# Kernel tuning notes

Measured on AMD Instinct MI355X. Metric: run time of the kernel, lower is better.

The kernel has to match this reference:

```python
import jax, jax.numpy as jnp
import numpy as np

# Dimensions
O, D, F_LSOA = 128, 128, 64      # origins, destinations, LSOA feature dim
T, FE, H = 128, 16, 64           # max seq len, edge_feature_dim, gru_hidden
NH, NO, PH = 128, 64, 128        # node_hidden, node_out, pair_hidden
P = O * D                        # number of O-D pairs


def _mlp3(x, W1, b1, W2, b2, W3, b3):
    # Linear->ReLU->Linear->ReLU->Linear (dropout is identity in eval mode)
    h = jax.nn.relu(x @ W1 + b1)
    h = jax.nn.relu(h @ W2 + b2)
    return h @ W3 + b3


def setup_inputs() -> dict:
    key = jax.random.key(0)
    ks = jax.random.split(key, 32)

    def rn(k, shape, s):
        return jax.random.normal(k, shape, dtype=jnp.float32) * s

    inp = {
        "O_feats": rn(ks[0], (O, F_LSOA), 1.0),
        "D_feats": rn(ks[1], (D, F_LSOA), 1.0),
        "seqs": rn(ks[2], (P, T, FE), 1.0),
        "lengths": jax.random.randint(ks[3], (P,), 1, T + 1, dtype=jnp.int32),
        # enc_O
        "WO1": rn(ks[4], (F_LSOA, NH), 0.05), "bO1": jnp.zeros((NH,), jnp.float32),
        "WO2": rn(ks[5], (NH, NH), 0.05),     "bO2": jnp.zeros((NH,), jnp.float32),
        "WO3": rn(ks[6], (NH, NO), 0.05),     "bO3": jnp.zeros((NO,), jnp.float32),
        # enc_D
        "WD1": rn(ks[7], (F_LSOA, NH), 0.05), "bD1": jnp.zeros((NH,), jnp.float32),
        "WD2": rn(ks[8], (NH, NH), 0.05),     "bD2": jnp.zeros((NH,), jnp.float32),
        "WD3": rn(ks[9], (NH, NO), 0.05),     "bD3": jnp.zeros((NO,), jnp.float32),
        # pair_head: 2*node_out -> pair_hidden -> 1
        "Wp1": rn(ks[10], (2 * NO, PH), 0.05), "bp1": jnp.zeros((PH,), jnp.float32),
        "Wp2": rn(ks[11], (PH, 1), 0.05),      "bp2": jnp.zeros((1,), jnp.float32),
        # GRU (gate order r, z, n as in PyTorch)
        "W_ih": rn(ks[12], (FE, 3 * H), 0.1),  "b_ih": jnp.zeros((3 * H,), jnp.float32),
        "W_hh": rn(ks[13], (H, 3 * H), 0.1),   "b_hh": jnp.zeros((3 * H,), jnp.float32),
        # seq_head
        "Ws": rn(ks[14], (H, 1), 0.1),         "bs": jnp.zeros((1,), jnp.float32),
    }
    return inp


def reference(O_feats, D_feats, seqs, lengths,
              WO1, bO1, WO2, bO2, WO3, bO3,
              WD1, bD1, WD2, bD2, WD3, bD3,
              Wp1, bp1, Wp2, bp2,
              W_ih, W_hh, b_ih, b_hh,
              Ws, bs):
    # Node encoders
    eo = _mlp3(O_feats, WO1, bO1, WO2, bO2, WO3, bO3)   # [O, NO]
    ed = _mlp3(D_feats, WD1, bD1, WD2, bD2, WD3, bD3)   # [D, NO]

    # Pairwise score: concat(eo, ed) -> MLP -> softplus
    pair_in = jnp.concatenate([
        jnp.broadcast_to(eo[:, None, :], (O, D, NO)),
        jnp.broadcast_to(ed[None, :, :], (O, D, NO)),
    ], axis=-1)                                          # [O, D, 2*NO]
    hp = jax.nn.relu(pair_in @ Wp1 + bp1)                # [O, D, PH]
    z_pair = (hp @ Wp2 + bp2)[..., 0]                    # [O, D]
    s_pair = jax.nn.softplus(z_pair)

    # Length-masked GRU over all O*D padded sequences (equiv. to pack_padded)
    xT = jnp.swapaxes(seqs, 0, 1)                        # [T, P, FE]
    h0 = jnp.zeros((P, H), jnp.float32)

    def step(h, inp):
        xt, t = inp
        gx = xt @ W_ih + b_ih                            # [P, 3H]
        gh = h @ W_hh + b_hh                             # [P, 3H]
        xr, xz, xn = jnp.split(gx, 3, axis=-1)
        hr, hz, hn = jnp.split(gh, 3, axis=-1)
        r = jax.nn.sigmoid(xr + hr)
        zg = jax.nn.sigmoid(xz + hz)
        n = jnp.tanh(xn + r * hn)
        h_new = (1.0 - zg) * n + zg * h
        h = jnp.where((t < lengths)[:, None], h_new, h)  # freeze past seq end
        return h, None

    h_last, _ = jax.lax.scan(step, h0, (xT, jnp.arange(T)))  # [P, H]

    p_seq = jax.nn.sigmoid(h_last @ Ws + bs)[:, 0].reshape(O, D)
    return jnp.sum(s_pair * p_seq)
```

## Files before the change

### kernel.cpp

```cpp
#include <hip/hip_runtime.h>
#include <hip/hip_bf16.h>

#define O_N 128
#define D_N 128
#define F_LS 64
#define T_MAX 128
#define FE_N 16
#define H_GRU 64
#define NH 128
#define NO 64
#define PH 128

typedef _Float16 f16;
typedef __fp16 hf2 __attribute__((ext_vector_type(2)));
typedef f16 f16x4 __attribute__((ext_vector_type(4)));
typedef f16 f16x8 __attribute__((ext_vector_type(8)));
typedef float f32x4 __attribute__((ext_vector_type(4)));

__device__ __forceinline__ float fast_sigmoid(float x) {
    return __builtin_amdgcn_rcpf(1.f + __expf(-x));
}

__global__ __launch_bounds__(256) void k_pre(
    const float* __restrict__ O_feats, const float* __restrict__ D_feats,
    const float* __restrict__ WO1, const float* __restrict__ bO1,
    const float* __restrict__ WO2, const float* __restrict__ bO2,
    const float* __restrict__ WO3, const float* __restrict__ bO3,
    const float* __restrict__ WD1, const float* __restrict__ bD1,
    const float* __restrict__ WD2, const float* __restrict__ bD2,
    const float* __restrict__ WD3, const float* __restrict__ bD3,
    const float* __restrict__ Wp1, const float* __restrict__ bp1,
    const int* __restrict__ lengths,
    float* __restrict__ PA, float* __restrict__ PBt,
    int* __restrict__ perm, float* __restrict__ d_out)
{
    const int t = threadIdx.x;
    if (blockIdx.x == 256) {
        __shared__ int cnt[130];
        __shared__ int suf[130];
        if (t < 130) cnt[t] = 0;
        __syncthreads();
        for (int i = t; i < 16384; i += 256) atomicAdd(&cnt[lengths[i]], 1);
        __syncthreads();
        if (t < 130) suf[t] = cnt[t];
        __syncthreads();
        for (int d = 1; d < 130; d <<= 1) {
            int v = 0;
            if (t < 130) { v = suf[t]; if (t + d < 130) v += suf[t + d]; }
            __syncthreads();
            if (t < 130) suf[t] = v;
            __syncthreads();
        }
        if (t < 129) cnt[t] = (t + 1 < 130) ? suf[t + 1] : 0;
        __syncthreads();
        for (int i = t; i < 16384; i += 256) {
            int pos = atomicAdd(&cnt[lengths[i]], 1);
            perm[pos] = i;
        }
        return;
    }

    __shared__ float h1[NH];
    __shared__ float h2[NH];
    __shared__ float ev[NO];
    const int b = blockIdx.x;
    const int enc = b >> 7;
    const int row = b & 127;
    if (b == 0 && t == 0) d_out[0] = 0.f;

    const float* x  = (enc ? D_feats : O_feats) + row * F_LS;
    const float* W1 = enc ? WD1 : WO1;  const float* b1 = enc ? bD1 : bO1;
    const float* W2 = enc ? WD2 : WO2;  const float* b2 = enc ? bD2 : bO2;
    const float* W3 = enc ? WD3 : WO3;  const float* b3 = enc ? bD3 : bO3;

    if (t < 128) {
        float a = b1[t];
        #pragma unroll 8
        for (int k = 0; k < F_LS; ++k) a += x[k] * W1[k * NH + t];
        h1[t] = fmaxf(a, 0.f);
    }
    __syncthreads();

    if (t < 128) {
        float a = b2[t];
        #pragma unroll 8
        for (int k = 0; k < NH; ++k) a += h1[k] * W2[k * NH + t];
        h2[t] = fmaxf(a, 0.f);
    }
    __syncthreads();

    if (t < NO) {
        float a = b3[t];
        #pragma unroll 8
        for (int k = 0; k < NH; ++k) a += h2[k] * W3[k * NO + t];
        ev[t] = a;
    }
    __syncthreads();

    if (t < 128) {
        const float* Wp = Wp1 + (enc ? NO * PH : 0);
        float a = 0.f;
        #pragma unroll 8
        for (int k = 0; k < NO; ++k) a += ev[k] * Wp[k * PH + t];
        if (enc) PBt[t * 128 + row] = a + bp1[t];
        else     PA[row * PH + t] = a;
    }
}

__global__ __launch_bounds__(256, 4) void k_gru(
    const float* __restrict__ seqs, const int* __restrict__ lengths,
    const int* __restrict__ perm,
    const float* __restrict__ W_ih, const float* __restrict__ b_ih,
    const float* __restrict__ W_hh, const float* __restrict__ b_hh,
    const float* __restrict__ Ws, const float* __restrict__ bs,
    const float* __restrict__ PA, const float* __restrict__ PBt,
    const float* __restrict__ Wp2, const float* __restrict__ bp2,
    float* __restrict__ d_out)
{
    __shared__ __align__(16) f16 hbuf[2][16 * 72];
    __shared__ __align__(16) float4 xbuf[2][8][64];
    __shared__ float red[64];
    const int tid = threadIdx.x;
    const int w  = tid >> 6;
    const int l  = tid & 63;
    const int q  = l >> 4;
    const int n  = l & 15;
    const int c  = w * 16 + n;
    const int colbase = w * 16 + q * 4;
    const int b2 = blockIdx.x & 255;
    const int j  = blockIdx.x >> 8;
    const int g  = (j == 0) ? 2 * b2
                 : (j == 1) ? 2 * b2 + 1
                 : (j == 2) ? 1022 - 2 * b2
                            : 1023 - 2 * b2;
    const int pb = g * 16;
    const float S_RZ = -1.4426950408889634f;
    const float S_N  =  2.8853900817779268f;

    f16x8 wh[3][2], wi[3];
    #pragma unroll
    for (int gg = 0; gg < 3; ++gg) {
        const int gb = gg * 64;
        const float s = (gg < 2) ? S_RZ : S_N;
        #pragma unroll
        for (int ks = 0; ks < 2; ++ks)
            #pragma unroll
            for (int jj = 0; jj < 8; ++jj)
                wh[gg][ks][jj] = (f16)(W_hh[(ks * 32 + q * 8 + jj) * 192 + gb + c] * s);
        #pragma unroll
        for (int jj = 0; jj < 8; ++jj) {
            int k = q * 8 + jj;
            wi[gg][jj] = (k < FE_N) ? (f16)(W_ih[k * 192 + gb + c] * s) : (f16)0.f;
        }
    }
    f32x4 c_r, c_z, c_hn, c_xn;
    float wsc[4];
    #pragma unroll
    for (int r = 0; r < 4; ++r) {
        int col = colbase + r;
        c_r[r]  = S_RZ * (b_ih[col] + b_hh[col]);
        c_z[r]  = S_RZ * (b_ih[64 + col] + b_hh[64 + col]);
        c_hn[r] = S_N * b_hh[128 + col];
        c_xn[r] = S_N * b_ih[128 + col];
        wsc[r]  = Ws[col];
    }
    const int myp   = perm[pb + n];
    const int mylen = lengths[myp];
    int ml = mylen;
    ml = max(ml, __shfl_xor(ml, 1));
    ml = max(ml, __shfl_xor(ml, 2));
    ml = max(ml, __shfl_xor(ml, 4));
    ml = max(ml, __shfl_xor(ml, 8));
    const int maxlen = __builtin_amdgcn_readfirstlane(ml);

    const float* xsrc = seqs + (size_t)perm[pb + (l & 15)] * (T_MAX * FE_N)
                       + (l >> 4) * 4;

    if (tid < 144) { f16x8 z8 = {}; *(f16x8*)&hbuf[0][tid * 8] = z8; }

    #pragma unroll
    for (int rr = 0; rr < 2; ++rr) {
        const int r8 = w + rr * 4;
        __builtin_amdgcn_global_load_lds(
            (const __attribute__((address_space(1))) void*)(xsrc + (size_t)r8 * FE_N),
            (__attribute__((address_space(3))) void*)&xbuf[0][r8][0], 16, 0, 0);
    }
    float hold[4] = {0.f, 0.f, 0.f, 0.f};
    const f16x8 zero8 = {};
    __syncthreads();

    #pragma unroll 1
    for (int t = 0; t < maxlen; ++t) {
        const int cur = t & 1;
        const int xb  = (t >> 3) & 1;
        const int row = t & 7;
        const f16* hb  = hbuf[cur];
        f16*       hbw = hbuf[cur ^ 1];
        f16x8 bh0 = *(const f16x8*)&hb[n * 72 + 8 * q];
        f16x8 bh1 = *(const f16x8*)&hb[n * 72 + 32 + 8 * q];

        if (row == 0 && t + 8 < maxlen) {
            const int nb = xb ^ 1;
            #pragma unroll
            for (int rr = 0; rr < 2; ++rr) {
                const int rl = w + rr * 4;
                int rg = t + 8 + rl;
                rg = rg < T_MAX ? rg : T_MAX - 1;
                __builtin_amdgcn_global_load_lds(
                    (const __attribute__((address_space(1))) void*)(xsrc + (size_t)rg * FE_N),
                    (__attribute__((address_space(3))) void*)&xbuf[nb][rl][0], 16, 0, 0);
            }
        }

        f16x8 ax = zero8;
        if (q < 2) {
            float4 a0 = xbuf[xb][row][32 * q + n];
            float4 a1 = xbuf[xb][row][32 * q + 16 + n];
            union { f16x8 v8; hf2 v2[4]; } u;
            u.v2[0] = __builtin_amdgcn_cvt_pkrtz(a0.x, a0.y);
            u.v2[1] = __builtin_amdgcn_cvt_pkrtz(a0.z, a0.w);
            u.v2[2] = __builtin_amdgcn_cvt_pkrtz(a1.x, a1.y);
            u.v2[3] = __builtin_amdgcn_cvt_pkrtz(a1.z, a1.w);
            ax = u.v8;
        }

        f32x4 ar = __builtin_amdgcn_mfma_f32_16x16x32_f16(wi[0], ax, c_r, 0, 0, 0);
        f32x4 az = __builtin_amdgcn_mfma_f32_16x16x32_f16(wi[1], ax, c_z, 0, 0, 0);
        f32x4 xn = __builtin_amdgcn_mfma_f32_16x16x32_f16(wi[2], ax, c_xn, 0, 0, 0);
        ar = __builtin_amdgcn_mfma_f32_16x16x32_f16(wh[0][0], bh0, ar, 0, 0, 0);
        ar = __builtin_amdgcn_mfma_f32_16x16x32_f16(wh[0][1], bh1, ar, 0, 0, 0);
        az = __builtin_amdgcn_mfma_f32_16x16x32_f16(wh[1][0], bh0, az, 0, 0, 0);
        az = __builtin_amdgcn_mfma_f32_16x16x32_f16(wh[1][1], bh1, az, 0, 0, 0);
        f32x4 hn = __builtin_amdgcn_mfma_f32_16x16x32_f16(wh[2][0], bh0, c_hn, 0, 0, 0);
        hn = __builtin_amdgcn_mfma_f32_16x16x32_f16(wh[2][1], bh1, hn, 0, 0, 0);

        const bool live = (t < mylen);
        #pragma unroll
        for (int r = 0; r < 4; ++r) {
            float rg    = __builtin_amdgcn_rcpf(1.f + __builtin_amdgcn_exp2f(ar[r]));
            float zg    = __builtin_amdgcn_rcpf(1.f + __builtin_amdgcn_exp2f(az[r]));
            float inner = fmaf(rg, hn[r], xn[r]);
            float nn    = fmaf(-2.f, __builtin_amdgcn_rcpf(1.f + __builtin_amdgcn_exp2f(inner)), 1.f);
            float hnew  = fmaf(zg, hold[r] - nn, nn);
            hold[r] = live ? hnew : hold[r];
        }
        union { f16x4 v4; hf2 v2[2]; } hu;
        hu.v2[0] = __builtin_amdgcn_cvt_pkrtz(hold[0], hold[1]);
        hu.v2[1] = __builtin_amdgcn_cvt_pkrtz(hold[2], hold[3]);
        *(f16x4*)&hbw[n * 72 + colbase] = hu.v4;
        __syncthreads();
    }

    float part = hold[0] * wsc[0] + hold[1] * wsc[1] +
                 hold[2] * wsc[2] + hold[3] * wsc[3];
    part += __shfl_xor(part, 16);
    part += __shfl_xor(part, 32);
    if (l < 16) red[w * 16 + n] = part;
    __syncthreads();

    const int pp = tid >> 4;
    const int u  = tid & 15;
    const int pidx = perm[pb + pp];
    const int ii = pidx >> 7;
    const int jj = pidx & 127;
    float acc = 0.f;
    #pragma unroll
    for (int cc = u; cc < PH; cc += 16)
        acc += Wp2[cc] * fmaxf(PA[ii * PH + cc] + PBt[cc * 128 + jj], 0.f);
    acc += __shfl_xor(acc, 1);
    acc += __shfl_xor(acc, 2);
    acc += __shfl_xor(acc, 4);
    acc += __shfl_xor(acc, 8);
    float contrib = 0.f;
    if (u == 0) {
        float z  = acc + bp2[0];
        float sp = fmaxf(z, 0.f) + log1pf(__expf(-fabsf(z)));
        float s  = red[pp] + red[16 + pp] + red[32 + pp] + red[48 + pp];
        float pv = fast_sigmoid(s + bs[0]);
        contrib  = sp * pv;
    }
    __syncthreads();
    if (u == 0) red[pp] = contrib;
    __syncthreads();
    if (tid == 0) {
        float tot = 0.f;
        #pragma unroll
        for (int k = 0; k < 16; ++k) tot += red[k];
        atomicAdd(d_out, tot);
    }
}

extern "C" void kernel_launch(void* const* d_in, const int* in_sizes, int n_in,
                              void* d_out, int out_size, void* d_ws, size_t ws_size,
                              hipStream_t stream)
{
    const float* O_feats = (const float*)d_in[0];
    const float* D_feats = (const float*)d_in[1];
    const float* seqs    = (const float*)d_in[2];
    const int*   lengths = (const int*)d_in[3];
    const float* WO1 = (const float*)d_in[4];  const float* bO1 = (const float*)d_in[5];
    const float* WO2 = (const float*)d_in[6];  const float* bO2 = (const float*)d_in[7];
    const float* WO3 = (const float*)d_in[8];  const float* bO3 = (const float*)d_in[9];
    const float* WD1 = (const float*)d_in[10]; const float* bD1 = (const float*)d_in[11];
    const float* WD2 = (const float*)d_in[12]; const float* bD2 = (const float*)d_in[13];
    const float* WD3 = (const float*)d_in[14]; const float* bD3 = (const float*)d_in[15];
    const float* Wp1 = (const float*)d_in[16]; const float* bp1 = (const float*)d_in[17];
    const float* Wp2 = (const float*)d_in[18]; const float* bp2 = (const float*)d_in[19];
    const float* W_ih = (const float*)d_in[20]; const float* b_ih = (const float*)d_in[21];
    const float* W_hh = (const float*)d_in[22]; const float* b_hh = (const float*)d_in[23];
    const float* Ws   = (const float*)d_in[24]; const float* bs   = (const float*)d_in[25];

    float* out    = (float*)d_out;
    float* PA     = (float*)d_ws;
    float* PBt    = PA + 128 * 128;
    int*   perm   = (int*)(PBt + 128 * 128);

    k_pre<<<257, 256, 0, stream>>>(O_feats, D_feats,
                                   WO1, bO1, WO2, bO2, WO3, bO3,
                                   WD1, bD1, WD2, bD2, WD3, bD3,
                                   Wp1, bp1, lengths, PA, PBt, perm, out);
    k_gru<<<1024, 256, 0, stream>>>(seqs, lengths, perm, W_ih, b_ih, W_hh, b_hh,
                                    Ws, bs, PA, PBt, Wp2, bp2, out);
}
```

Baseline: 341.6 us.

## Convert GRU kernel to persistent blocks pulling length-sorted groups from an atomic queue

The GRU kernel becomes persistent. 512 blocks repeatedly claim 16-sequence groups from a global atomic counter, which k_pre resets. Because perm is sorted by descending length, this gives dynamic longest-first scheduling. Each group's maxlen is read from its first element instead of a shuffle reduction, and per-pair results go straight to the output with atomicAdd, replacing the per-block reduction. The aim is load balancing across uneven sequence lengths. In exchange, far fewer blocks are resident to hide recurrence latency, and there are more global atomics.

```diff
diff --git a/kernel.cpp b/kernel.cpp
--- a/kernel.cpp
+++ b/kernel.cpp
@@ -10,6 +10,7 @@
 #define NH 128
 #define NO 64
 #define PH 128
+#define NGRP 1024
 
 typedef _Float16 f16;
 typedef __fp16 hf2 __attribute__((ext_vector_type(2)));
@@ -32,12 +33,13 @@
     const float* __restrict__ Wp1, const float* __restrict__ bp1,
     const int* __restrict__ lengths,
     float* __restrict__ PA, float* __restrict__ PBt,
-    int* __restrict__ perm, float* __restrict__ d_out)
+    int* __restrict__ perm, int* __restrict__ gcnt, float* __restrict__ d_out)
 {
     const int t = threadIdx.x;
     if (blockIdx.x == 256) {
         __shared__ int cnt[130];
         __shared__ int suf[130];
+        if (t == 0) gcnt[0] = 0;
         if (t < 130) cnt[t] = 0;
         __syncthreads();
         for (int i = t; i < 16384; i += 256) atomicAdd(&cnt[lengths[i]], 1);
@@ -109,7 +111,7 @@
 
 __global__ __launch_bounds__(256, 4) void k_gru(
     const float* __restrict__ seqs, const int* __restrict__ lengths,
-    const int* __restrict__ perm,
+    const int* __restrict__ perm, int* __restrict__ gcnt,
     const float* __restrict__ W_ih, const float* __restrict__ b_ih,
     const float* __restrict__ W_hh, const float* __restrict__ b_hh,
     const float* __restrict__ Ws, const float* __restrict__ bs,
@@ -120,6 +122,7 @@
     __shared__ __align__(16) f16 hbuf[2][16 * 72];
     __shared__ __align__(16) float4 xbuf[2][8][64];
     __shared__ float red[64];
+    __shared__ int sg;
     const int tid = threadIdx.x;
     const int w  = tid >> 6;
     const int l  = tid & 63;
@@ -127,13 +130,6 @@
     const int n  = l & 15;
     const int c  = w * 16 + n;
     const int colbase = w * 16 + q * 4;
-    const int b2 = blockIdx.x & 255;
-    const int j  = blockIdx.x >> 8;
-    const int g  = (j == 0) ? 2 * b2
-                 : (j == 1) ? 2 * b2 + 1
-                 : (j == 2) ? 1022 - 2 * b2
-                            : 1023 - 2 * b2;
-    const int pb = g * 16;
     const float S_RZ = -1.4426950408889634f;
     const float S_N  =  2.8853900817779268f;
 
@@ -164,129 +160,123 @@
         c_xn[r] = S_N * b_ih[128 + col];
         wsc[r]  = Ws[col];
     }
-    const int myp   = perm[pb + n];
-    const int mylen = lengths[myp];
-    int ml = mylen;
-    ml = max(ml, __shfl_xor(ml, 1));
-    ml = max(ml, __shfl_xor(ml, 2));
-    ml = max(ml, __shfl_xor(ml, 4));
-    ml = max(ml, __shfl_xor(ml, 8));
-    const int maxlen = __builtin_amdgcn_readfirstlane(ml);
-
-    const float* xsrc = seqs + (size_t)perm[pb + (l & 15)] * (T_MAX * FE_N)
-                       + (l >> 4) * 4;
-
-    if (tid < 144) { f16x8 z8 = {}; *(f16x8*)&hbuf[0][tid * 8] = z8; }
-
-    #pragma unroll
-    for (int rr = 0; rr < 2; ++rr) {
-        const int r8 = w + rr * 4;
-        __builtin_amdgcn_global_load_lds(
-            (const __attribute__((address_space(1))) void*)(xsrc + (size_t)r8 * FE_N),
-            (__attribute__((address_space(3))) void*)&xbuf[0][r8][0], 16, 0, 0);
-    }
-    float hold[4] = {0.f, 0.f, 0.f, 0.f};
     const f16x8 zero8 = {};
-    __syncthreads();
-
-    #pragma unroll 1
-    for (int t = 0; t < maxlen; ++t) {
-        const int cur = t & 1;
-        const int xb  = (t >> 3) & 1;
-        const int row = t & 7;
-        const f16* hb  = hbuf[cur];
-        f16*       hbw = hbuf[cur ^ 1];
-        f16x8 bh0 = *(const f16x8*)&hb[n * 72 + 8 * q];
-        f16x8 bh1 = *(const f16x8*)&hb[n * 72 + 32 + 8 * q];
-
-        if (row == 0 && t + 8 < maxlen) {
-            const int nb = xb ^ 1;
+
+    for (;;) {
+        if (tid == 0) sg = atomicAdd(gcnt, 1);
+        __syncthreads();
+        const int g = sg;
+        if (g >= NGRP) break;
+        const int pb = g * 16;
+
+        const int myp   = perm[pb + n];
+        const int mylen = lengths[myp];
+        const int maxlen = lengths[perm[pb]];
+
+        const float* xsrc = seqs + (size_t)perm[pb + (l & 15)] * (T_MAX * FE_N)
+                           + (l >> 4) * 4;
+
+        if (tid < 144) { f16x8 z8 = {}; *(f16x8*)&hbuf[0][tid * 8] = z8; }
+
+        #pragma unroll
+        for (int rr = 0; rr < 2; ++rr) {
+            const int r8 = w + rr * 4;
+            __builtin_amdgcn_global_load_lds(
+                (const __attribute__((address_space(1))) void*)(xsrc + (size_t)r8 * FE_N),
+                (__attribute__((address_space(3))) void*)&xbuf[0][r8][0], 16, 0, 0);
+        }
+        float hold[4] = {0.f, 0.f, 0.f, 0.f};
+        __syncthreads();
+
+        #pragma unroll 1
+        for (int t = 0; t < maxlen; ++t) {
+            const int cur = t & 1;
+            const int xb  = (t >> 3) & 1;
+            const int row = t & 7;
+            const f16* hb  = hbuf[cur];
+            f16*       hbw = hbuf[cur ^ 1];
+            f16x8 bh0 = *(const f16x8*)&hb[n * 72 + 8 * q];
+            f16x8 bh1 = *(const f16x8*)&hb[n * 72 + 32 + 8 * q];
+
+            if (row == 0 && t + 8 < maxlen) {
+                const int nb = xb ^ 1;
+                #pragma unroll
+                for (int rr = 0; rr < 2; ++rr) {
+                    const int rl = w + rr * 4;
+                    int rg = t + 8 + rl;
+                    rg = rg < T_MAX ? rg : T_MAX - 1;
+                    __builtin_amdgcn_global_load_lds(
+                        (const __attribute__((address_space(1))) void*)(xsrc + (size_t)rg * FE_N),
+                        (__attribute__((address_space(3))) void*)&xbuf[nb][rl][0], 16, 0, 0);
+                }
+            }
+
+            f16x8 ax = zero8;
+            if (q < 2) {
+                float4 a0 = xbuf[xb][row][32 * q + n];
+                float4 a1 = xbuf[xb][row][32 * q + 16 + n];
+                union { f16x8 v8; hf2 v2[4]; } u;
+                u.v2[0] = __builtin_amdgcn_cvt_pkrtz(a0.x, a0.y);
+                u.v2[1] = __builtin_amdgcn_cvt_pkrtz(a0.z, a0.w);
+                u.v2[2] = __builtin_amdgcn_cvt_pkrtz(a1.x, a1.y);
+                u.v2[3] = __builtin_amdgcn_cvt_pkrtz(a1.z, a1.w);
+                ax = u.v8;
+            }
+
+            f32x4 ar = __builtin_amdgcn_mfma_f32_16x16x32_f16(wi[0], ax, c_r, 0, 0, 0);
+            f32x4 az = __builtin_amdgcn_mfma_f32_16x16x32_f16(wi[1], ax, c_z, 0, 0, 0);
+            f32x4 xn = __builtin_amdgcn_mfma_f32_16x16x32_f16(wi[2], ax, c_xn, 0, 0, 0);
+            ar = __builtin_amdgcn_mfma_f32_16x16x32_f16(wh[0][0], bh0, ar, 0, 0, 0);
+            ar = __builtin_amdgcn_mfma_f32_16x16x32_f16(wh[0][1], bh1, ar, 0, 0, 0);
+            az = __builtin_amdgcn_mfma_f32_16x16x32_f16(wh[1][0], bh0, az, 0, 0, 0);
+            az = __builtin_amdgcn_mfma_f32_16x16x32_f16(wh[1][1], bh1, az, 0, 0, 0);
+            f32x4 hn = __builtin_amdgcn_mfma_f32_16x16x32_f16(wh[2][0], bh0, c_hn, 0, 0, 0);
+            hn = __builtin_amdgcn_mfma_f32_16x16x32_f16(wh[2][1], bh1, hn, 0, 0, 0);
+
+            const bool live = (t < mylen);
             #pragma unroll
-            for (int rr = 0; rr < 2; ++rr) {
-                const int rl = w + rr * 4;
-                int rg = t + 8 + rl;
-                rg = rg < T_MAX ? rg : T_MAX - 1;
-                __builtin_amdgcn_global_load_lds(
-                    (const __attribute__((address_space(1))) void*)(xsrc + (size_t)rg * FE_N),
-                    (__attribute__((address_space(3))) void*)&xbuf[nb][rl][0], 16, 0, 0);
+            for (int r = 0; r < 4; ++r) {
+                float rg    = __builtin_amdgcn_rcpf(1.f + __builtin_amdgcn_exp2f(ar[r]));
+                float zg    = __builtin_amdgcn_rcpf(1.f + __builtin_amdgcn_exp2f(az[r]));
+                float inner = fmaf(rg, hn[r], xn[r]);
+                float nn    = fmaf(-2.f, __builtin_amdgcn_rcpf(1.f + __builtin_amdgcn_exp2f(inner)), 1.f);
+                float hnew  = fmaf(zg, hold[r] - nn, nn);
+                hold[r] = live ? hnew : hold[r];
             }
-        }
-
-        f16x8 ax = zero8;
-        if (q < 2) {
-            float4 a0 = xbuf[xb][row][32 * q + n];
-            float4 a1 = xbuf[xb][row][32 * q + 16 + n];
-            union { f16x8 v8; hf2 v2[4]; } u;
-            u.v2[0] = __builtin_amdgcn_cvt_pkrtz(a0.x, a0.y);
-            u.v2[1] = __builtin_amdgcn_cvt_pkrtz(a0.z, a0.w);
-            u.v2[2] = __builtin_amdgcn_cvt_pkrtz(a1.x, a1.y);
-            u.v2[3] = __builtin_amdgcn_cvt_pkrtz(a1.z, a1.w);
-            ax = u.v8;
-        }
-
-        f32x4 ar = __builtin_amdgcn_mfma_f32_16x16x32_f16(wi[0], ax, c_r, 0, 0, 0);
-        f32x4 az = __builtin_amdgcn_mfma_f32_16x16x32_f16(wi[1], ax, c_z, 0, 0, 0);
-        f32x4 xn = __builtin_amdgcn_mfma_f32_16x16x32_f16(wi[2], ax, c_xn, 0, 0, 0);
-        ar = __builtin_amdgcn_mfma_f32_16x16x32_f16(wh[0][0], bh0, ar, 0, 0, 0);
-        ar = __builtin_amdgcn_mfma_f32_16x16x32_f16(wh[0][1], bh1, ar, 0, 0, 0);
-        az = __builtin_amdgcn_mfma_f32_16x16x32_f16(wh[1][0], bh0, az, 0, 0, 0);
-        az = __builtin_amdgcn_mfma_f32_16x16x32_f16(wh[1][1], bh1, az, 0, 0, 0);
-        f32x4 hn = __builtin_amdgcn_mfma_f32_16x16x32_f16(wh[2][0], bh0, c_hn, 0, 0, 0);
-        hn = __builtin_amdgcn_mfma_f32_16x16x32_f16(wh[2][1], bh1, hn, 0, 0, 0);
-
-        const bool live = (t < mylen);
+            union { f16x4 v4; hf2 v2[2]; } hu;
+            hu.v2[0] = __builtin_amdgcn_cvt_pkrtz(hold[0], hold[1]);
+            hu.v2[1] = __builtin_amdgcn_cvt_pkrtz(hold[2], hold[3]);
+            *(f16x4*)&hbw[n * 72 + colbase] = hu.v4;
+            __syncthreads();
+        }
+
+        float part = hold[0] * wsc[0] + hold[1] * wsc[1] +
+                     hold[2] * wsc[2] + hold[3] * wsc[3];
+        part += __shfl_xor(part, 16);
+        part += __shfl_xor(part, 32);
+        if (l < 16) red[w * 16 + n] = part;
+        __syncthreads();
+
+        const int pp = tid >> 4;
+        const int u  = tid & 15;
+        const int pidx = perm[pb + pp];
+        const int ii = pidx >> 7;
+        const int jj = pidx & 127;
+        float acc = 0.f;
         #pragma unroll
-        for (int r = 0; r < 4; ++r) {
-            float rg    = __builtin_amdgcn_rcpf(1.f + __builtin_amdgcn_exp2f(ar[r]));
-            float zg    = __builtin_amdgcn_rcpf(1.f + __builtin_amdgcn_exp2f(az[r]));
-            float inner = fmaf(rg, hn[r], xn[r]);
-            float nn    = fmaf(-2.f, __builtin_amdgcn_rcpf(1.f + __builtin_amdgcn_exp2f(inner)), 1.f);
-            float hnew  = fmaf(zg, hold[r] - nn, nn);
-            hold[r] = live ? hnew : hold[r];
-        }
-        union { f16x4 v4; hf2 v2[2]; } hu;
-        hu.v2[0] = __builtin_amdgcn_cvt_pkrtz(hold[0], hold[1]);
-        hu.v2[1] = __builtin_amdgcn_cvt_pkrtz(hold[2], hold[3]);
-        *(f16x4*)&hbw[n * 72 + colbase] = hu.v4;
-        __syncthreads();
-    }
-
-    float part = hold[0] * wsc[0] + hold[1] * wsc[1] +
-                 hold[2] * wsc[2] + hold[3] * wsc[3];
-    part += __shfl_xor(part, 16);
-    part += __shfl_xor(part, 32);
-    if (l < 16) red[w * 16 + n] = part;
-    __syncthreads();
-
-    const int pp = tid >> 4;
-    const int u  = tid & 15;
-    const int pidx = perm[pb + pp];
-    const int ii = pidx >> 7;
-    const int jj = pidx & 127;
-    float acc = 0.f;
-    #pragma unroll
-    for (int cc = u; cc < PH; cc += 16)
-        acc += Wp2[cc] * fmaxf(PA[ii * PH + cc] + PBt[cc * 128 + jj], 0.f);
-    acc += __shfl_xor(acc, 1);
-    acc += __shfl_xor(acc, 2);
-    acc += __shfl_xor(acc, 4);
-    acc += __shfl_xor(acc, 8);
-    float contrib = 0.f;
-    if (u == 0) {
-        float z  = acc + bp2[0];
-        float sp = fmaxf(z, 0.f) + log1pf(__expf(-fabsf(z)));
-        float s  = red[pp] + red[16 + pp] + red[32 + pp] + red[48 + pp];
-        float pv = fast_sigmoid(s + bs[0]);
-        contrib  = sp * pv;
-    }
-    __syncthreads();
-    if (u == 0) red[pp] = contrib;
-    __syncthreads();
-    if (tid == 0) {
-        float tot = 0.f;
-        #pragma unroll
-        for (int k = 0; k < 16; ++k) tot += red[k];
-        atomicAdd(d_out, tot);
+        for (int cc = u; cc < PH; cc += 16)
+            acc += Wp2[cc] * fmaxf(PA[ii * PH + cc] + PBt[cc * 128 + jj], 0.f);
+        acc += __shfl_xor(acc, 1);
+        acc += __shfl_xor(acc, 2);
+        acc += __shfl_xor(acc, 4);
+        acc += __shfl_xor(acc, 8);
+        if (u == 0) {
+            float z  = acc + bp2[0];
+            float sp = fmaxf(z, 0.f) + log1pf(__expf(-fabsf(z)));
+            float s  = red[pp] + red[16 + pp] + red[32 + pp] + red[48 + pp];
+            float pv = fast_sigmoid(s + bs[0]);
+            atomicAdd(d_out, sp * pv);
+        }
     }
 }
 
@@ -314,11 +304,12 @@
     float* PA     = (float*)d_ws;
     float* PBt    = PA + 128 * 128;
     int*   perm   = (int*)(PBt + 128 * 128);
+    int*   gcnt   = perm + 16384;
 
     k_pre<<<257, 256, 0, stream>>>(O_feats, D_feats,
                                    WO1, bO1, WO2, bO2, WO3, bO3,
                                    WD1, bD1, WD2, bD2, WD3, bD3,
-                                   Wp1, bp1, lengths, PA, PBt, perm, out);
-    k_gru<<<1024, 256, 0, stream>>>(seqs, lengths, perm, W_ih, b_ih, W_hh, b_hh,
-                                    Ws, bs, PA, PBt, Wp2, bp2, out);
+                                   Wp1, bp1, lengths, PA, PBt, perm, gcnt, out);
+    k_gru<<<512, 256, 0, stream>>>(seqs, lengths, perm, gcnt, W_ih, b_ih,
+                                   W_hh, b_hh, Ws, bs, PA, PBt, Wp2, bp2, out);
 }
```

New measurement: 369.0 us. 1.08x slower.
